# Kernel tuning notes

Hardware: AMD Instinct MI355X
Metric: run time of the kernel (lower is better)

## Reference

```python
import jax, jax.numpy as jnp
import numpy as np

# Coefficients expressing each of the 16 soft binary logic gates as
# c0 + ca*a + cb*b + cab*(a*b), in standard difflogic op order:
# 0:False 1:AND 2:a&~b 3:A 4:~a&b 5:B 6:XOR 7:OR 8:NOR 9:XNOR
# 10:~B 11:B=>A 12:~A 13:A=>B 14:NAND 15:True
GATE_COEF = jnp.array([
    [0, 0, 0, 0],
    [0, 0, 0, 1],
    [0, 1, 0, -1],
    [0, 1, 0, 0],
    [0, 0, 1, -1],
    [0, 0, 1, 0],
    [0, 1, 1, -2],
    [0, 1, 1, -1],
    [1, -1, -1, 1],
    [1, -1, -1, 2],
    [1, 0, -1, 0],
    [1, 0, -1, 1],
    [1, -1, 0, 0],
    [1, -1, 0, 1],
    [1, 0, 0, -1],
    [1, 0, 0, 0],
], dtype=jnp.float32)  # [16, 4]

INPUT_DIM = 8192
HIDDEN_DIMS = [16384, 16384, 16384, 16384]
OUTPUT_DIM = 1000
BATCH = 2048
TAU = 1.0
N_GATES = 16


def setup_inputs() -> dict:
    key = jax.random.key(0)
    kx, key = jax.random.split(key)
    inp = {"x": jax.random.uniform(kx, (BATCH, INPUT_DIM), dtype=jnp.float32)}
    dims = [INPUT_DIM] + HIDDEN_DIMS + [OUTPUT_DIM]
    for i in range(len(dims) - 1):
        in_d, out_d = dims[i], dims[i + 1]
        kw, ka, kb, key = jax.random.split(key, 4)
        inp[f"w{i}"] = jax.random.normal(kw, (out_d, N_GATES), dtype=jnp.float32)
        inp[f"ia{i}"] = jax.random.randint(ka, (out_d,), 0, in_d, dtype=jnp.int32)
        inp[f"ib{i}"] = jax.random.randint(kb, (out_d,), 0, in_d, dtype=jnp.int32)
    return inp


def _logic_layer(x, w, ia, ib):
    # gather the two inputs of every neuron: [batch, out_dim]
    a = x[:, ia]
    b = x[:, ib]
    p = jax.nn.softmax(w, axis=-1)              # [out_dim, 16]
    coef = p @ GATE_COEF                         # [out_dim, 4]
    # weighted mixture of all 16 gates, fused via bilinear form
    return coef[:, 0] + coef[:, 1] * a + coef[:, 2] * b + coef[:, 3] * (a * b)


def reference(x, w0, w1, w2, w3, w4, ia0, ia1, ia2, ia3, ia4, ib0, ib1, ib2, ib3, ib4):
    ws = [w0, w1, w2, w3, w4]
    ias = [ia0, ia1, ia2, ia3, ia4]
    ibs = [ib0, ib1, ib2, ib3, ib4]
    h = x
    for w, ia, ib in zip(ws, ias, ibs):
        h = _logic_layer(h, w, ia, ib)
    # GroupSum(output_dim, tau): split last dim into output_dim groups, sum, /tau
    batch = h.shape[0]
    group = h.shape[-1] // OUTPUT_DIM
    out = h.reshape(batch, OUTPUT_DIM, group).sum(-1) / TAU
    return out
```

## Files before the change

### kernel.cpp

```cpp
#include <hip/hip_runtime.h>


#define NBATCH 2048
#define IN_DIM 8192
#define HID 16384
#define OUT_DIM 1000
#define LDS_ENT 18432
#define MARKV 0x7FFFFFFF

typedef __attribute__((ext_vector_type(4))) _Float16 half4;
typedef __attribute__((ext_vector_type(2))) _Float16 half2v;

__device__ __constant__ float GC_dev[64] = {
    0, 0, 0, 0,   0, 0, 0, 1,   0, 1, 0, -1,  0, 1, 0, 0,
    0, 0, 1, -1,  0, 0, 1, 0,   0, 1, 1, -2,  0, 1, 1, -1,
    1, -1, -1, 1, 1, -1, -1, 2, 1, 0, -1, 0,  1, 0, -1, 1,
    1, -1, 0, 0,  1, -1, 0, 1,  1, 0, 0, -1,  1, 0, 0, 0
};

struct Tabs {
    const float* w[5];
    const int* ia[5];
    const int* ib[5];
};

__device__ __forceinline__ half4 coef_of(const float* __restrict__ wrow) {
    float v[16];
    const float4* w4 = (const float4*)wrow;
#pragma unroll
    for (int i = 0; i < 4; ++i) {
        float4 t = w4[i];
        v[4*i+0] = t.x; v[4*i+1] = t.y; v[4*i+2] = t.z; v[4*i+3] = t.w;
    }
    float m = v[0];
#pragma unroll
    for (int g = 1; g < 16; ++g) m = fmaxf(m, v[g]);
    float s = 0.f;
#pragma unroll
    for (int g = 0; g < 16; ++g) { v[g] = __expf(v[g] - m); s += v[g]; }
    float inv = 1.f / s;
    float c0 = 0.f, c1 = 0.f, c2 = 0.f, c3 = 0.f;
#pragma unroll
    for (int g = 0; g < 16; ++g) {
        c0 += v[g] * GC_dev[g*4+0];
        c1 += v[g] * GC_dev[g*4+1];
        c2 += v[g] * GC_dev[g*4+2];
        c3 += v[g] * GC_dev[g*4+3];
    }
    half4 c;
    c[0] = (_Float16)(c0*inv); c[1] = (_Float16)(c1*inv);
    c[2] = (_Float16)(c2*inv); c[3] = (_Float16)(c3*inv);
    return c;
}

__global__ __launch_bounds__(256) void mark_out_kernel(
    const int* __restrict__ ia4, const int* __restrict__ ib4,
    int* __restrict__ map3, int* __restrict__ header) {
    int t = blockIdx.x * 256 + threadIdx.x;
    if (t < 16) header[t] = 0;
    if (t < OUT_DIM) { map3[ia4[t]] = MARKV; map3[ib4[t]] = MARKV; }
}

__global__ __launch_bounds__(256) void assign_mark_kernel(
    int* __restrict__ mapl, int* __restrict__ mapm1,
    const int* __restrict__ ia, const int* __restrict__ ib,
    int* __restrict__ counter) {
    int i = blockIdx.x * 256 + threadIdx.x;
    if (mapl[i] == MARKV) {
        mapl[i] = atomicAdd(counter, 1);
        if (mapm1) { mapm1[ia[i]] = MARKV; mapm1[ib[i]] = MARKV; }
    }
}

__global__ __launch_bounds__(256) void build_all_kernel(
    Tabs args, const int* __restrict__ map0, const int* __restrict__ map1,
    const int* __restrict__ map2, const int* __restrict__ map3,
    unsigned int* __restrict__ tabIdx, half4* __restrict__ tabCoef) {
    int i = blockIdx.x * 256 + threadIdx.x;

    if (i < OUT_DIM) {
        unsigned a = (unsigned)map3[args.ia[4][i]];
        unsigned b = (unsigned)map3[args.ib[4][i]];
        tabIdx[4*HID + i] = a | (b << 16);
        tabCoef[4*HID + i] = coef_of(args.w[4] + (size_t)i * 16);
    }
    int s3 = map3[i];
    if (s3 >= 0) {
        unsigned a = 8192u + (unsigned)map2[args.ia[3][i]];
        unsigned b = 8192u + (unsigned)map2[args.ib[3][i]];
        tabIdx[3*HID + s3] = a | (b << 16);
        tabCoef[3*HID + s3] = coef_of(args.w[3] + (size_t)i * 16);
    }
    int s2 = map2[i];
    if (s2 >= 0) {
        unsigned a = (unsigned)map1[args.ia[2][i]];
        unsigned b = (unsigned)map1[args.ib[2][i]];
        tabIdx[2*HID + s2] = a | (b << 16);
        tabCoef[2*HID + s2] = coef_of(args.w[2] + (size_t)i * 16);
    }
    int s1 = map1[i];
    if (s1 >= 0) {
        unsigned a = 8192u + (unsigned)map0[args.ia[1][i]];
        unsigned b = 8192u + (unsigned)map0[args.ib[1][i]];
        tabIdx[1*HID + s1] = a | (b << 16);
        tabCoef[1*HID + s1] = coef_of(args.w[1] + (size_t)i * 16);
    }
    int s0 = map0[i];
    if (s0 >= 0) {
        tabIdx[0*HID + s0] =
            (unsigned)args.ia[0][i] | ((unsigned)args.ib[0][i] << 16);
        tabCoef[0*HID + s0] = coef_of(args.w[0] + (size_t)i * 16);
    }
}

__device__ __forceinline__ void layer_pass(
    half2v* lds, const unsigned* __restrict__ tIdx,
    const half4* __restrict__ tCoef, int n, int wbase, int t) {
    for (int j = t; j < n; j += 1024) {
        unsigned idx = tIdx[j];
        half4 c = tCoef[j];
        half2v pa = lds[idx & 0xFFFFu];
        half2v pb = lds[idx >> 16];
        float c0 = (float)c[0], c1 = (float)c[1];
        float c2 = (float)c[2], c3 = (float)c[3];
        float a0 = (float)pa[0], a1 = (float)pa[1];
        float q0 = (float)pb[0], q1 = (float)pb[1];
        half2v o;
        o[0] = (_Float16)fmaf(fmaf(c3, q0, c1), a0, fmaf(c2, q0, c0));
        o[1] = (_Float16)fmaf(fmaf(c3, q1, c1), a1, fmaf(c2, q1, c0));
        lds[wbase + j] = o;
    }
    __syncthreads();
}

__global__ __launch_bounds__(1024) void fused_kernel(
    const float* __restrict__ x, const unsigned* __restrict__ tabIdx,
    const half4* __restrict__ tabCoef, const int* __restrict__ header,
    float* __restrict__ out) {
    extern __shared__ half2v lds[];
    int bp = blockIdx.x;
    int t = threadIdx.x;
    int b0 = 2 * bp, b1 = 2 * bp + 1;
    int n0 = header[0], n1 = header[1], n2 = header[2], n3 = header[3];

    const float4* xr0 = (const float4*)(x + (size_t)b0 * IN_DIM);
    const float4* xr1 = (const float4*)(x + (size_t)b1 * IN_DIM);
#pragma unroll
    for (int i = 0; i < 2; ++i) {
        int e = i * 1024 + t;
        float4 v0 = xr0[e];
        float4 v1 = xr1[e];
        half2v h0; h0[0] = (_Float16)v0.x; h0[1] = (_Float16)v1.x;
        half2v h1; h1[0] = (_Float16)v0.y; h1[1] = (_Float16)v1.y;
        half2v h2; h2[0] = (_Float16)v0.z; h2[1] = (_Float16)v1.z;
        half2v h3; h3[0] = (_Float16)v0.w; h3[1] = (_Float16)v1.w;
        lds[4*e+0] = h0; lds[4*e+1] = h1; lds[4*e+2] = h2; lds[4*e+3] = h3;
    }
    __syncthreads();

    layer_pass(lds, tabIdx + 0*HID, tabCoef + 0*HID, n0, 8192, t);
    layer_pass(lds, tabIdx + 1*HID, tabCoef + 1*HID, n1, 0,    t);
    layer_pass(lds, tabIdx + 2*HID, tabCoef + 2*HID, n2, 8192, t);
    layer_pass(lds, tabIdx + 3*HID, tabCoef + 3*HID, n3, 0,    t);

    if (t < OUT_DIM) {
        unsigned idx = tabIdx[4*HID + t];
        half4 c = tabCoef[4*HID + t];
        half2v pa = lds[idx & 0xFFFFu];
        half2v pb = lds[idx >> 16];
        float c0 = (float)c[0], c1 = (float)c[1];
        float c2 = (float)c[2], c3 = (float)c[3];
        float a0 = (float)pa[0], a1 = (float)pa[1];
        float q0 = (float)pb[0], q1 = (float)pb[1];
        out[(size_t)b0 * OUT_DIM + t] = fmaf(fmaf(c3, q0, c1), a0, fmaf(c2, q0, c0));
        out[(size_t)b1 * OUT_DIM + t] = fmaf(fmaf(c3, q1, c1), a1, fmaf(c2, q1, c0));
    }
}

extern "C" void kernel_launch(void* const* d_in, const int* in_sizes, int n_in,
                              void* d_out, int out_size, void* d_ws, size_t ws_size,
                              hipStream_t stream) {
    Tabs args;
    const float* x = (const float*)d_in[0];
    for (int i = 0; i < 5; ++i) {
        args.w[i]  = (const float*)d_in[1 + 3 * i];
        args.ia[i] = (const int*)d_in[2 + 3 * i];
        args.ib[i] = (const int*)d_in[3 + 3 * i];
    }

    char* ws = (char*)d_ws;
    int* maps = (int*)ws;
    int* header = (int*)(ws + 4 * HID * 4);
    unsigned int* tabIdx = (unsigned int*)(ws + 4*HID*4 + 64);
    half4* tabCoef = (half4*)(ws + 4*HID*4 + 64 + 5*HID*4);
    int* map0 = maps, *map1 = maps + HID, *map2 = maps + 2*HID, *map3 = maps + 3*HID;

    hipMemsetAsync(maps, 0xFF, 4 * HID * 4, stream);

    mark_out_kernel<<<(OUT_DIM + 255) / 256, 256, 0, stream>>>(
        args.ia[4], args.ib[4], map3, header);
    assign_mark_kernel<<<HID / 256, 256, 0, stream>>>(
        map3, map2, args.ia[3], args.ib[3], header + 3);
    assign_mark_kernel<<<HID / 256, 256, 0, stream>>>(
        map2, map1, args.ia[2], args.ib[2], header + 2);
    assign_mark_kernel<<<HID / 256, 256, 0, stream>>>(
        map1, map0, args.ia[1], args.ib[1], header + 1);
    assign_mark_kernel<<<HID / 256, 256, 0, stream>>>(
        map0, (int*)nullptr, args.ia[0], args.ib[0], header + 0);
    build_all_kernel<<<HID / 256, 256, 0, stream>>>(
        args, map0, map1, map2, map3, tabIdx, tabCoef);
    fused_kernel<<<NBATCH / 2, 1024, LDS_ENT * sizeof(half2v), stream>>>(
        x, tabIdx, tabCoef, header, (float*)d_out);
}
```

Baseline: 166.4 us.

## Merge table-building launches into one kernel with software grid barriers

Replaces the memset plus five small mark/assign kernels and the build kernel with a single 64-block kernel that uses atomic-counter grid barriers between the backward liveness passes. This removes several kernel launch gaps in the preprocessing chain. It relies on all 64 blocks being co-resident and adds spin-wait barrier overhead; the header memset is kept to reset counters and the barrier.

```diff
diff --git a/kernel.cpp b/kernel.cpp
--- a/kernel.cpp
+++ b/kernel.cpp
@@ -53,30 +53,51 @@
     return c;
 }
 
-__global__ __launch_bounds__(256) void mark_out_kernel(
-    const int* __restrict__ ia4, const int* __restrict__ ib4,
-    int* __restrict__ map3, int* __restrict__ header) {
-    int t = blockIdx.x * 256 + threadIdx.x;
-    if (t < 16) header[t] = 0;
-    if (t < OUT_DIM) { map3[ia4[t]] = MARKV; map3[ib4[t]] = MARKV; }
-}
-
-__global__ __launch_bounds__(256) void assign_mark_kernel(
-    int* __restrict__ mapl, int* __restrict__ mapm1,
-    const int* __restrict__ ia, const int* __restrict__ ib,
-    int* __restrict__ counter) {
-    int i = blockIdx.x * 256 + threadIdx.x;
-    if (mapl[i] == MARKV) {
-        mapl[i] = atomicAdd(counter, 1);
-        if (mapm1) { mapm1[ia[i]] = MARKV; mapm1[ib[i]] = MARKV; }
-    }
-}
-
-__global__ __launch_bounds__(256) void build_all_kernel(
-    Tabs args, const int* __restrict__ map0, const int* __restrict__ map1,
-    const int* __restrict__ map2, const int* __restrict__ map3,
+__device__ __forceinline__ void gridbar(int* bar, int target) {
+    __syncthreads();
+    if (threadIdx.x == 0) {
+        __threadfence();
+        __hip_atomic_fetch_add(bar, 1, __ATOMIC_ACQ_REL, __HIP_MEMORY_SCOPE_AGENT);
+        while (__hip_atomic_load(bar, __ATOMIC_ACQUIRE, __HIP_MEMORY_SCOPE_AGENT) < target) {
+            __builtin_amdgcn_s_sleep(1);
+        }
+        __threadfence();
+    }
+    __syncthreads();
+}
+
+__global__ __launch_bounds__(256) void super_build_kernel(
+    Tabs args, int* __restrict__ maps, int* __restrict__ header,
     unsigned int* __restrict__ tabIdx, half4* __restrict__ tabCoef) {
     int i = blockIdx.x * 256 + threadIdx.x;
+    int* map0 = maps, *map1 = maps + HID, *map2 = maps + 2*HID, *map3 = maps + 3*HID;
+    int* bar = header + 8;
+
+    map0[i] = -1; map1[i] = -1; map2[i] = -1; map3[i] = -1;
+    gridbar(bar, 64);
+
+    if (i < OUT_DIM) { map3[args.ia[4][i]] = MARKV; map3[args.ib[4][i]] = MARKV; }
+    gridbar(bar, 128);
+
+    if (map3[i] == MARKV) {
+        map3[i] = atomicAdd(header + 3, 1);
+        map2[args.ia[3][i]] = MARKV; map2[args.ib[3][i]] = MARKV;
+    }
+    gridbar(bar, 192);
+    if (map2[i] == MARKV) {
+        map2[i] = atomicAdd(header + 2, 1);
+        map1[args.ia[2][i]] = MARKV; map1[args.ib[2][i]] = MARKV;
+    }
+    gridbar(bar, 256);
+    if (map1[i] == MARKV) {
+        map1[i] = atomicAdd(header + 1, 1);
+        map0[args.ia[1][i]] = MARKV; map0[args.ib[1][i]] = MARKV;
+    }
+    gridbar(bar, 320);
+    if (map0[i] == MARKV) {
+        map0[i] = atomicAdd(header + 0, 1);
+    }
+    gridbar(bar, 384);
 
     if (i < OUT_DIM) {
         unsigned a = (unsigned)map3[args.ia[4][i]];
@@ -193,22 +214,9 @@
     int* header = (int*)(ws + 4 * HID * 4);
     unsigned int* tabIdx = (unsigned int*)(ws + 4*HID*4 + 64);
     half4* tabCoef = (half4*)(ws + 4*HID*4 + 64 + 5*HID*4);
-    int* map0 = maps, *map1 = maps + HID, *map2 = maps + 2*HID, *map3 = maps + 3*HID;
-
-    hipMemsetAsync(maps, 0xFF, 4 * HID * 4, stream);
-
-    mark_out_kernel<<<(OUT_DIM + 255) / 256, 256, 0, stream>>>(
-        args.ia[4], args.ib[4], map3, header);
-    assign_mark_kernel<<<HID / 256, 256, 0, stream>>>(
-        map3, map2, args.ia[3], args.ib[3], header + 3);
-    assign_mark_kernel<<<HID / 256, 256, 0, stream>>>(
-        map2, map1, args.ia[2], args.ib[2], header + 2);
-    assign_mark_kernel<<<HID / 256, 256, 0, stream>>>(
-        map1, map0, args.ia[1], args.ib[1], header + 1);
-    assign_mark_kernel<<<HID / 256, 256, 0, stream>>>(
-        map0, (int*)nullptr, args.ia[0], args.ib[0], header + 0);
-    build_all_kernel<<<HID / 256, 256, 0, stream>>>(
-        args, map0, map1, map2, map3, tabIdx, tabCoef);
+
+    hipMemsetAsync(header, 0, 64, stream);
+    super_build_kernel<<<64, 256, 0, stream>>>(args, maps, header, tabIdx, tabCoef);
     fused_kernel<<<NBATCH / 2, 1024, LDS_ENT * sizeof(half2v), stream>>>(
         x, tabIdx, tabCoef, header, (float*)d_out);
 }
```

New measurement: 186.5 us. 12.1% more time.
